# Performance work log

Measured on AMD Instinct MI355X. Metric: run time of the kernel, lower is better.

## Reference

```python
import jax, jax.numpy as jnp
import numpy as np

B, T, L = 128, 1024, 96


def setup_inputs() -> dict:
    key = jax.random.key(0)
    k1, k2, k3 = jax.random.split(key, 3)
    inputs = jax.random.normal(k1, (B, T, L), dtype=jnp.float32)
    labels_idx = jax.random.randint(k2, (B, T), 0, L, dtype=jnp.int32)
    trans = jax.random.normal(k3, (L, L), dtype=jnp.float32) * 0.1
    return {"inputs": inputs, "labels_idx": labels_idx, "trans": trans}


def reference(inputs, labels_idx, trans):
    # inputs: [B,T,L] emission scores; trans: [L,L]; labels_idx: [B,T] ints
    num_labels = trans.shape[0]
    labels = jax.nn.one_hot(labels_idx, num_labels, dtype=inputs.dtype)  # [B,T,L]

    # --- log partition via forward algorithm (sequential logsumexp scan) ---
    init = inputs[:, 0]  # [B,L]

    def step(state, x_t):
        # state: [B,L] alpha; trans[i,j] = score of i -> j
        new = jax.scipy.special.logsumexp(state[:, :, None] + trans[None, :, :], axis=1) + x_t
        return new, None

    xs = jnp.swapaxes(inputs[:, 1:], 0, 1)  # [T-1,B,L]
    final, _ = jax.lax.scan(step, init, xs)  # [B,L]
    log_norm = jax.scipy.special.logsumexp(final, axis=1, keepdims=True)  # [B,1]

    # --- gold path score ---
    point_score = jnp.sum(inputs * labels, axis=(1, 2))[:, None]  # [B,1]
    trans_score = jnp.einsum('btl,btm,lm->b', labels[:, :-1], labels[:, 1:], trans)[:, None]  # [B,1]

    return log_norm - (point_score + trans_score)  # [B,1] NLL per sequence
```

## Files before the change

kernel.cpp:

```cpp
#include <hip/hip_runtime.h>
#include <math.h>

#define Bb 128
#define Tt 1024
#define Ll 96
#define NSEG 16
#define DELTA 24
#define CUT(s) (1 + ((Tt - 1) * (s)) / NSEG)

#define WS_STRIDE 80

typedef float v2f __attribute__((ext_vector_type(2)));
typedef float v4f __attribute__((ext_vector_type(4)));
typedef int   v2i __attribute__((ext_vector_type(2)));

static __device__ __forceinline__ float xadd32(float p) {
#if __has_builtin(__builtin_amdgcn_permlane32_swap)
    v2i rr = __builtin_amdgcn_permlane32_swap(__float_as_int(p),
                                              __float_as_int(p), false, false);
    return __int_as_float(rr.x) + __int_as_float(rr.y);
#else
    return p + __shfl_xor(p, 32, 64);
#endif
}

__global__ __launch_bounds__(64, 1)
void crf_scan_kernel(
    const float* __restrict__ inputs,
    const int*   __restrict__ labels_idx,
    const float* __restrict__ trans,
    float*       __restrict__ ws)
{
    const int cid = blockIdx.x / Bb;
    const int b   = blockIdx.x % Bb;
    const int i   = threadIdx.x;

    const float* xbase = inputs + (size_t)b * Tt * Ll;
    float* wsb = ws + (size_t)b * WS_STRIDE;
    int*   wsi = reinterpret_cast<int*>(wsb);

    if (cid == NSEG) {
        float ps = 0.f;
        const int* lb = labels_idx + b * Tt;
        #pragma unroll 4
        for (int t = i; t < Tt; t += 64) {
            int i0 = lb[t];
            ps += xbase[t * Ll + i0];
            if (t < Tt - 1) ps += trans[i0 * Ll + lb[t + 1]];
        }
        #pragma unroll
        for (int off = 32; off; off >>= 1) ps += __shfl_xor(ps, off, 64);
        if (i == 0) wsb[4 * NSEG] = ps;
        return;
    }

    const int s  = cid + 1;
    const int lo = CUT(s - 1), hi = CUT(s);
    const int w0 = (s == 1) ? 1 : ((lo - DELTA < 1) ? 1 : lo - DELTA);
    const int jt = (s == 1) ? 0 : (lo - 1);

    const int g   = i >> 5;
    const int j   = i & 31;
    const int g48 = g * 48;
    const int cA  = j, cB = j + 32, cC = j + 64;

    __shared__ __align__(16) float buf[Ll];

#define EP24(X) \
    X(0)  X(1)  X(2)  X(3)  X(4)  X(5)  X(6)  X(7)  X(8)  X(9)  X(10) X(11) \
    X(12) X(13) X(14) X(15) X(16) X(17) X(18) X(19) X(20) X(21) X(22) X(23)

#define EDECL(p) v2f EA##p, EB##p, EC##p;
    EP24(EDECL)
#undef EDECL
#define EINIT(p) { \
        int e0 = (g48 + 2*(p)) * Ll, e1 = (g48 + 2*(p) + 1) * Ll; \
        EA##p = (v2f){__expf(trans[e0 + cA]), __expf(trans[e1 + cA])}; \
        EB##p = (v2f){__expf(trans[e0 + cB]), __expf(trans[e1 + cB])}; \
        EC##p = (v2f){__expf(trans[e0 + cC]), __expf(trans[e1 + cC])}; \
        asm volatile("" ::: "memory"); }
    EP24(EINIT)
#undef EINIT

#define CHUNK(q, p0, p1) { \
        aA0 += (v2f){P##q.x, P##q.y} * EA##p0; \
        aA1 += (v2f){P##q.z, P##q.w} * EA##p1; \
        aB0 += (v2f){P##q.x, P##q.y} * EB##p0; \
        aB1 += (v2f){P##q.z, P##q.w} * EB##p1; \
        aC0 += (v2f){P##q.x, P##q.y} * EC##p0; \
        aC1 += (v2f){P##q.z, P##q.w} * EC##p1; }

#define MATVEC \
        CHUNK(0, 0, 1)   CHUNK(1, 2, 3)   CHUNK(2, 4, 5)   CHUNK(3, 6, 7)   \
        CHUNK(4, 8, 9)   CHUNK(5, 10,11)  CHUNK(6, 12,13)  CHUNK(7, 14,15)  \
        CHUNK(8, 16,17)  CHUNK(9, 18,19)  CHUNK(10,20,21)  CHUNK(11,22,23)

#define PRELOAD { const v4f* qb_ = reinterpret_cast<const v4f*>(buf) + g * 12; \
        P0 = qb_[0]; P1 = qb_[1]; P2  = qb_[2];  P3  = qb_[3];  \
        P4 = qb_[4]; P5 = qb_[5]; P6  = qb_[6];  P7  = qb_[7];  \
        P8 = qb_[8]; P9 = qb_[9]; P10 = qb_[10]; P11 = qb_[11]; \
        Pk = buf[0]; }

    v4f P0,P1,P2,P3,P4,P5,P6,P7,P8,P9,P10,P11;
    float Pk;

    float qA = __expf(xbase[(w0 - 1) * Ll + cA]);
    float qB = __expf(xbase[(w0 - 1) * Ll + cB]);
    float qC = __expf(xbase[(w0 - 1) * Ll + cC]);
    if (i < 32) { buf[cA] = qA; buf[cB] = qB; buf[cC] = qC; }
    asm volatile("" ::: "memory");
    PRELOAD

    float ewA = __expf(xbase[w0 * Ll + cA]);
    float ewB = __expf(xbase[w0 * Ll + cB]);
    float ewC = __expf(xbase[w0 * Ll + cC]);
#define ROWF(d) ((w0 + (d) > Tt - 1) ? (Tt - 1) : (w0 + (d)))
    float x2A = xbase[ROWF(1)*Ll+cA], x2B = xbase[ROWF(1)*Ll+cB], x2C = xbase[ROWF(1)*Ll+cC];
    float x3A = xbase[ROWF(2)*Ll+cA], x3B = xbase[ROWF(2)*Ll+cB], x3C = xbase[ROWF(2)*Ll+cC];
    float x4A = xbase[ROWF(3)*Ll+cA], x4B = xbase[ROWF(3)*Ll+cB], x4C = xbase[ROWF(3)*Ll+cC];
    float x5A = xbase[ROWF(4)*Ll+cA], x5B = xbase[ROWF(4)*Ll+cB], x5C = xbase[ROWF(4)*Ll+cC];
    float x6A = xbase[ROWF(5)*Ll+cA], x6B = xbase[ROWF(5)*Ll+cB], x6C = xbase[ROWF(5)*Ll+cC];
    float x7A = xbase[ROWF(6)*Ll+cA], x7B = xbase[ROWF(6)*Ll+cB], x7C = xbase[ROWF(6)*Ll+cC];
#undef ROWF

    int Dk = 0;
    float jsum = 1.f; int jdk = 0;
    #pragma unroll 1
    for (int t = w0; t < hi; ++t) {
        int k = ((__float_as_int(Pk) >> 23) & 0xff) - 127;
        Dk += k;
        float r = __uint_as_float((unsigned)(127 - k) << 23);
        float wA = ewA * r, wB = ewB * r, wC = ewC * r;

        v2f aA0 = {0.f,0.f}, aA1 = {0.f,0.f};
        v2f aB0 = {0.f,0.f}, aB1 = {0.f,0.f};
        v2f aC0 = {0.f,0.f}, aC1 = {0.f,0.f};
        MATVEC
        v2f tA = aA0 + aA1, tB = aB0 + aB1, tC = aC0 + aC1;
        qA = xadd32(tA.x + tA.y) * wA;
        qB = xadd32(tB.x + tB.y) * wB;
        qC = xadd32(tC.x + tC.y) * wC;

        if (i < 32) { buf[cA] = qA; buf[cB] = qB; buf[cC] = qC; }
        asm volatile("" ::: "memory");
        PRELOAD

        if (t == jt) {
            float ssum = qA + qB + qC;
            #pragma unroll
            for (int off = 16; off; off >>= 1) ssum += __shfl_xor(ssum, off, 64);
            jsum = ssum; jdk = Dk;
        }

        ewA = __expf(x2A); ewB = __expf(x2B); ewC = __expf(x2C);
        x2A = x3A; x2B = x3B; x2C = x3C;
        x3A = x4A; x3B = x4B; x3C = x4C;
        x4A = x5A; x4B = x5B; x4C = x5C;
        x5A = x6A; x5B = x6B; x5C = x6C;
        x6A = x7A; x6B = x7B; x6C = x7C;
        int row = t + 7; if (row > Tt - 1) row = Tt - 1;
        x7A = xbase[row*Ll+cA]; x7B = xbase[row*Ll+cB]; x7C = xbase[row*Ll+cC];
    }

    float esum = qA + qB + qC;
    #pragma unroll
    for (int off = 16; off; off >>= 1) esum += __shfl_xor(esum, off, 64);

    if (i == 0) {
        wsb[s - 1]            = esum;
        wsb[NSEG + s - 1]     = jsum;
        wsi[2 * NSEG + s - 1] = Dk;
        wsi[3 * NSEG + s - 1] = jdk;
    }
#undef PRELOAD
#undef MATVEC
#undef CHUNK
#undef EP24
}

__global__ __launch_bounds__(64, 1) void crf_combine_kernel(
    const float* __restrict__ ws, float* __restrict__ out)
{
    const int b = blockIdx.x;
    if (threadIdx.x != 0) return;
    const float* wsb = ws + (size_t)b * WS_STRIDE;
    const int*   wsi = reinterpret_cast<const int*>(wsb);
    const double LN2 = 0.6931471805599453;

    double acc = 0.0;
    #pragma unroll 1
    for (int s = 1; s <= NSEG; ++s) {
        acc += log((double)wsb[s - 1]) + LN2 * (double)wsi[2 * NSEG + s - 1];
        if (s >= 2)
            acc -= log((double)wsb[NSEG + s - 1]) + LN2 * (double)wsi[3 * NSEG + s - 1];
    }
    out[b] = (float)(acc - (double)wsb[4 * NSEG]);
}

extern "C" void kernel_launch(void* const* d_in, const int* in_sizes, int n_in,
                              void* d_out, int out_size, void* d_ws, size_t ws_size,
                              hipStream_t stream) {
    const float* inputs     = (const float*)d_in[0];
    const int*   labels_idx = (const int*)d_in[1];
    const float* trans      = (const float*)d_in[2];
    float*       out        = (float*)d_out;
    float*       ws         = (float*)d_ws;

    crf_scan_kernel<<<dim3((NSEG + 1) * Bb), dim3(64), 0, stream>>>(
        inputs, labels_idx, trans, ws);
    crf_combine_kernel<<<dim3(Bb), dim3(64), 0, stream>>>(ws, out);
}
```

Baseline: 147.1 us.

## Fuse combine into scan via atomic counter and use fewer, longer segments

Removes the separate combine kernel. Each scan block now bumps a per-batch atomic counter after writing its partial results, and the last block to arrive computes the final NLL; a memset zeroes the counters before launch. The number of time segments drops from 16 to 12 and the overlap warmup from 24 to 16, which cuts the block count but lengthens each block's serial chain. The emission prefetch depth also drops from 7 rows to 4, saving registers at the risk of exposing load latency.

```diff
diff --git a/kernel.cpp b/kernel.cpp
--- a/kernel.cpp
+++ b/kernel.cpp
@@ -4,11 +4,11 @@
 #define Bb 128
 #define Tt 1024
 #define Ll 96
-#define NSEG 16
-#define DELTA 24
+#define NSEG 12
+#define DELTA 16
 #define CUT(s) (1 + ((Tt - 1) * (s)) / NSEG)
 
-#define WS_STRIDE 80
+#define WS_STRIDE 64
 
 typedef float v2f __attribute__((ext_vector_type(2)));
 typedef float v4f __attribute__((ext_vector_type(4)));
@@ -24,12 +24,26 @@
 #endif
 }
 
+static __device__ void combine_batch(const float* wsb, float* out, int b) {
+    const int* wsi = reinterpret_cast<const int*>(wsb);
+    const double LN2 = 0.6931471805599453;
+    double acc = 0.0;
+    #pragma unroll 1
+    for (int s = 1; s <= NSEG; ++s) {
+        acc += log((double)wsb[s - 1]) + LN2 * (double)wsi[2 * NSEG + s - 1];
+        if (s >= 2)
+            acc -= log((double)wsb[NSEG + s - 1]) + LN2 * (double)wsi[3 * NSEG + s - 1];
+    }
+    out[b] = (float)(acc - (double)wsb[4 * NSEG]);
+}
+
 __global__ __launch_bounds__(64, 1)
 void crf_scan_kernel(
     const float* __restrict__ inputs,
     const int*   __restrict__ labels_idx,
     const float* __restrict__ trans,
-    float*       __restrict__ ws)
+    float*       __restrict__ ws,
+    float*       __restrict__ out)
 {
     const int cid = blockIdx.x / Bb;
     const int b   = blockIdx.x % Bb;
@@ -38,6 +52,7 @@
     const float* xbase = inputs + (size_t)b * Tt * Ll;
     float* wsb = ws + (size_t)b * WS_STRIDE;
     int*   wsi = reinterpret_cast<int*>(wsb);
+    int*   cnt = reinterpret_cast<int*>(ws + (size_t)Bb * WS_STRIDE);
 
     if (cid == NSEG) {
         float ps = 0.f;
@@ -50,7 +65,12 @@
         }
         #pragma unroll
         for (int off = 32; off; off >>= 1) ps += __shfl_xor(ps, off, 64);
-        if (i == 0) wsb[4 * NSEG] = ps;
+        if (i == 0) {
+            wsb[4 * NSEG] = ps;
+            __threadfence();
+            int old = atomicAdd(&cnt[b], 1);
+            if (old == NSEG) { __threadfence(); combine_batch(wsb, out, b); }
+        }
         return;
     }
 
@@ -118,9 +138,6 @@
     float x2A = xbase[ROWF(1)*Ll+cA], x2B = xbase[ROWF(1)*Ll+cB], x2C = xbase[ROWF(1)*Ll+cC];
     float x3A = xbase[ROWF(2)*Ll+cA], x3B = xbase[ROWF(2)*Ll+cB], x3C = xbase[ROWF(2)*Ll+cC];
     float x4A = xbase[ROWF(3)*Ll+cA], x4B = xbase[ROWF(3)*Ll+cB], x4C = xbase[ROWF(3)*Ll+cC];
-    float x5A = xbase[ROWF(4)*Ll+cA], x5B = xbase[ROWF(4)*Ll+cB], x5C = xbase[ROWF(4)*Ll+cC];
-    float x6A = xbase[ROWF(5)*Ll+cA], x6B = xbase[ROWF(5)*Ll+cB], x6C = xbase[ROWF(5)*Ll+cC];
-    float x7A = xbase[ROWF(6)*Ll+cA], x7B = xbase[ROWF(6)*Ll+cB], x7C = xbase[ROWF(6)*Ll+cC];
 #undef ROWF
 
     int Dk = 0;
@@ -155,11 +172,8 @@
         ewA = __expf(x2A); ewB = __expf(x2B); ewC = __expf(x2C);
         x2A = x3A; x2B = x3B; x2C = x3C;
         x3A = x4A; x3B = x4B; x3C = x4C;
-        x4A = x5A; x4B = x5B; x4C = x5C;
-        x5A = x6A; x5B = x6B; x5C = x6C;
-        x6A = x7A; x6B = x7B; x6C = x7C;
-        int row = t + 7; if (row > Tt - 1) row = Tt - 1;
-        x7A = xbase[row*Ll+cA]; x7B = xbase[row*Ll+cB]; x7C = xbase[row*Ll+cC];
+        int row = t + 4; if (row > Tt - 1) row = Tt - 1;
+        x4A = xbase[row*Ll+cA]; x4B = xbase[row*Ll+cB]; x4C = xbase[row*Ll+cC];
     }
 
     float esum = qA + qB + qC;
@@ -171,30 +185,17 @@
         wsb[NSEG + s - 1]     = jsum;
         wsi[2 * NSEG + s - 1] = Dk;
         wsi[3 * NSEG + s - 1] = jdk;
+        __threadfence();
+        int old = atomicAdd(&cnt[b], 1);
+        if (old == NSEG) {
+            __threadfence();
+            combine_batch(wsb, out, b);
+        }
     }
 #undef PRELOAD
 #undef MATVEC
 #undef CHUNK
 #undef EP24
-}
-
-__global__ __launch_bounds__(64, 1) void crf_combine_kernel(
-    const float* __restrict__ ws, float* __restrict__ out)
-{
-    const int b = blockIdx.x;
-    if (threadIdx.x != 0) return;
-    const float* wsb = ws + (size_t)b * WS_STRIDE;
-    const int*   wsi = reinterpret_cast<const int*>(wsb);
-    const double LN2 = 0.6931471805599453;
-
-    double acc = 0.0;
-    #pragma unroll 1
-    for (int s = 1; s <= NSEG; ++s) {
-        acc += log((double)wsb[s - 1]) + LN2 * (double)wsi[2 * NSEG + s - 1];
-        if (s >= 2)
-            acc -= log((double)wsb[NSEG + s - 1]) + LN2 * (double)wsi[3 * NSEG + s - 1];
-    }
-    out[b] = (float)(acc - (double)wsb[4 * NSEG]);
 }
 
 extern "C" void kernel_launch(void* const* d_in, const int* in_sizes, int n_in,
@@ -206,7 +207,8 @@
     float*       out        = (float*)d_out;
     float*       ws         = (float*)d_ws;
 
+    hipMemsetAsync((char*)d_ws + (size_t)Bb * WS_STRIDE * sizeof(float), 0,
+                   Bb * sizeof(int), stream);
     crf_scan_kernel<<<dim3((NSEG + 1) * Bb), dim3(64), 0, stream>>>(
-        inputs, labels_idx, trans, ws);
-    crf_combine_kernel<<<dim3(Bb), dim3(64), 0, stream>>>(ws, out);
-}
+        inputs, labels_idx, trans, ws, out);
+}
```

After: 169.3 us. 1.15x slower.
